# Kernel tuning notes

Measured on AMD Instinct MI355X. Metric: run time of the kernel, lower is better.

## Reference

```python
import jax, jax.numpy as jnp
import numpy as np

D_MODEL = 512
NUM_HEADS = 8
D_K = D_MODEL // NUM_HEADS
SCALE = D_K ** (-0.5)
B, L = 2, 256


def _tropical_linear(x, W, b):
    # max-plus linear: y[..., o] = max_i (x[..., i] + W[o, i]) + b[o]
    # x: (B, L, Din), W: (Dout, Din)
    return jnp.max(x[:, :, None, :] + W[None, None, :, :], axis=-1) + b


def _split_heads(t):
    Bn, Ln, Dn = t.shape
    return t.reshape(Bn, Ln, NUM_HEADS, D_K).transpose(0, 2, 1, 3)  # (B,H,L,dk)


def setup_inputs() -> dict:
    key = jax.random.key(0)
    ks = jax.random.split(key, 8)
    s = 1.0 / np.sqrt(D_MODEL)
    return {
        "x": jax.random.normal(ks[0], (B, L, D_MODEL), jnp.float32),
        "qW": jax.random.normal(ks[1], (D_MODEL, D_MODEL), jnp.float32) * s,
        "qb": jnp.zeros((D_MODEL,), jnp.float32),
        "kW": jax.random.normal(ks[2], (D_MODEL, D_MODEL), jnp.float32) * s,
        "kb": jnp.zeros((D_MODEL,), jnp.float32),
        "vW": jax.random.normal(ks[3], (D_MODEL, D_MODEL), jnp.float32) * s,
        "vb": jnp.zeros((D_MODEL,), jnp.float32),
        "oW": jax.random.normal(ks[4], (D_MODEL, D_MODEL), jnp.float32) * s,
        "ob": jnp.zeros((D_MODEL,), jnp.float32),
        "gW": jnp.zeros((NUM_HEADS, D_MODEL), jnp.float32),  # torch init: zeros
        "gb": jnp.full((NUM_HEADS,), 2.0, jnp.float32),      # torch init: +2.0
        "temp": jnp.ones((NUM_HEADS,), jnp.float32),
    }


def reference(x, qW, qb, kW, kb, vW, vb, oW, ob, gW, gb, temp):
    Bn, Ln, Dn = x.shape
    Q = _split_heads(_tropical_linear(x, qW, qb))  # (B,H,L,dk)
    K = _split_heads(_tropical_linear(x, kW, kb))
    V = _split_heads(x @ vW.T + vb)

    class_scores = jnp.einsum('bhqd,bhkd->bhqk', Q, K) * SCALE
    # tropical max-plus scores: max_d (Q[q,d] + K[k,d])
    trop_scores = jnp.max(Q[:, :, :, None, :] + K[:, :, None, :, :], axis=-1) * SCALE

    g = jax.nn.sigmoid(x @ gW.T + gb)            # (B,L,H)
    g = g.transpose(0, 2, 1)[..., None]          # (B,H,L,1)
    scores = g * trop_scores + (1.0 - g) * class_scores

    # Maslov temperature softmax: per-head learnable temperature
    attn = jax.nn.softmax(scores / temp[None, :, None, None], axis=-1)

    out = jnp.einsum('bhqk,bhkd->bhqd', attn, V)
    out = out.transpose(0, 2, 1, 3).reshape(Bn, Ln, Dn)
    return out @ oW.T + ob, attn
```

## Files before the change

### kernel.cpp

```cpp
#include <hip/hip_runtime.h>
#include <math.h>

#define DM    512
#define LSEQ  256
#define NB    2
#define NH    8
#define DK    64
#define SCALEF 0.125f
#define KC    64

__global__ __launch_bounds__(256) void qkvg_kernel(
    const float* __restrict__ x,
    const float* __restrict__ qW, const float* __restrict__ kW,
    const float* __restrict__ vW,
    const float* __restrict__ gW, const float* __restrict__ gb,
    float* __restrict__ P1, float* __restrict__ go)
{
    const int tid = threadIdx.x;
    const int bx  = blockIdx.x;

    if (bx >= 768) {
        const int gx  = bx - 768;
        const int row = gx * 32 + (tid >> 3);
        const int h   = tid & 7;
        const float4* xr = (const float4*)(x  + row * DM);
        const float4* wr = (const float4*)(gW + h  * DM);
        float acc = 0.f;
        #pragma unroll 8
        for (int i = 0; i < DM / 4; ++i) {
            float4 a = xr[i], w = wr[i];
            acc = fmaf(a.x, w.x, acc);
            acc = fmaf(a.y, w.y, acc);
            acc = fmaf(a.z, w.z, acc);
            acc = fmaf(a.w, w.w, acc);
        }
        acc += gb[h];
        go[row * NH + h] = 1.f / (1.f + __expf(-acc));
        return;
    }

    const int ks = bx & 3;
    const int t  = bx >> 2;
    const int rt = t / 24;
    const int ct = t % 24;
    const int op = ct >> 3;
    const int row0  = rt * 64;
    const int col0m = (ct & 7) * 64;
    const int kbase = ks * 128;

    const float* __restrict__ W = (op == 0) ? qW : (op == 1) ? kW : vW;
    const bool trop = (op < 2);

    __shared__ float Xs[KC][68];
    __shared__ float Ws[KC][68];

    const int ty = tid >> 4, tx = tid & 15;
    const int sr = tid & 63;
    const int sq = tid >> 6;

    const float* xp = x + (row0  + sr) * DM + kbase + sq * 16;
    const float* wp = W + (col0m + sr) * DM + kbase + sq * 16;

    float4 xg[4], wg[4];
    #pragma unroll
    for (int i = 0; i < 4; ++i) {
        xg[i] = *(const float4*)(xp + i * 4);
        wg[i] = *(const float4*)(wp + i * 4);
    }

    const float init = trop ? -INFINITY : 0.f;
    float acc[4][4];
    #pragma unroll
    for (int i = 0; i < 4; ++i)
        #pragma unroll
        for (int j = 0; j < 4; ++j) acc[i][j] = init;

    #pragma unroll
    for (int k0 = 0; k0 < 128; k0 += KC) {
        __syncthreads();
        #pragma unroll
        for (int i = 0; i < 4; ++i) {
            const int kk = sq * 16 + i * 4;
            Xs[kk + 0][sr] = xg[i].x;  Xs[kk + 1][sr] = xg[i].y;
            Xs[kk + 2][sr] = xg[i].z;  Xs[kk + 3][sr] = xg[i].w;
            Ws[kk + 0][sr] = wg[i].x;  Ws[kk + 1][sr] = wg[i].y;
            Ws[kk + 2][sr] = wg[i].z;  Ws[kk + 3][sr] = wg[i].w;
        }
        __syncthreads();
        if (k0 + KC < 128) {
            #pragma unroll
            for (int i = 0; i < 4; ++i) {
                xg[i] = *(const float4*)(xp + KC + i * 4);
                wg[i] = *(const float4*)(wp + KC + i * 4);
            }
        }
        if (trop) {
            #pragma unroll 4
            for (int kp = 0; kp < KC / 2; ++kp) {
                const int kk = kp * 2;
                float4 x0 = *(const float4*)&Xs[kk    ][ty * 4];
                float4 x1 = *(const float4*)&Xs[kk + 1][ty * 4];
                float4 w0 = *(const float4*)&Ws[kk    ][tx * 4];
                float4 w1 = *(const float4*)&Ws[kk + 1][tx * 4];
                const float xa0[4] = {x0.x, x0.y, x0.z, x0.w};
                const float xa1[4] = {x1.x, x1.y, x1.z, x1.w};
                const float wa0[4] = {w0.x, w0.y, w0.z, w0.w};
                const float wa1[4] = {w1.x, w1.y, w1.z, w1.w};
                #pragma unroll
                for (int i = 0; i < 4; ++i)
                    #pragma unroll
                    for (int j = 0; j < 4; ++j)
                        acc[i][j] = fmaxf(fmaxf(acc[i][j], xa0[i] + wa0[j]),
                                          xa1[i] + wa1[j]);
            }
        } else {
            #pragma unroll 4
            for (int kp = 0; kp < KC / 2; ++kp) {
                const int kk = kp * 2;
                float4 x0 = *(const float4*)&Xs[kk    ][ty * 4];
                float4 x1 = *(const float4*)&Xs[kk + 1][ty * 4];
                float4 w0 = *(const float4*)&Ws[kk    ][tx * 4];
                float4 w1 = *(const float4*)&Ws[kk + 1][tx * 4];
                const float xa0[4] = {x0.x, x0.y, x0.z, x0.w};
                const float xa1[4] = {x1.x, x1.y, x1.z, x1.w};
                const float wa0[4] = {w0.x, w0.y, w0.z, w0.w};
                const float wa1[4] = {w1.x, w1.y, w1.z, w1.w};
                #pragma unroll
                for (int i = 0; i < 4; ++i)
                    #pragma unroll
                    for (int j = 0; j < 4; ++j) {
                        acc[i][j] = fmaf(xa0[i], wa0[j], acc[i][j]);
                        acc[i][j] = fmaf(xa1[i], wa1[j], acc[i][j]);
                    }
            }
        }
    }

    const int gcol = op * 512 + col0m + tx * 4;
    #pragma unroll
    for (int i = 0; i < 4; ++i) {
        const int r = row0 + ty * 4 + i;
        *(float4*)&P1[((size_t)ks * 512 + r) * 1536 + gcol] =
            make_float4(acc[i][0], acc[i][1], acc[i][2], acc[i][3]);
    }
}

__global__ __launch_bounds__(256) void qkv_reduce_kernel(
    const float* __restrict__ P1,
    const float* __restrict__ qb, const float* __restrict__ kb,
    const float* __restrict__ vb,
    float* __restrict__ Qo, float* __restrict__ Ko, float* __restrict__ Vo)
{
    const int e   = blockIdx.x * 256 + threadIdx.x;
    const int row = e / 384;
    const int col = (e % 384) * 4;
    const size_t base = (size_t)row * 1536 + col;

    float4 p0 = *(const float4*)&P1[base];
    float4 p1 = *(const float4*)&P1[base +  786432];
    float4 p2 = *(const float4*)&P1[base + 1572864];
    float4 p3 = *(const float4*)&P1[base + 2359296];

    if (col < 1024) {
        float4 r = make_float4(
            fmaxf(fmaxf(p0.x, p1.x), fmaxf(p2.x, p3.x)),
            fmaxf(fmaxf(p0.y, p1.y), fmaxf(p2.y, p3.y)),
            fmaxf(fmaxf(p0.z, p1.z), fmaxf(p2.z, p3.z)),
            fmaxf(fmaxf(p0.w, p1.w), fmaxf(p2.w, p3.w)));
        if (col < 512) {
            float4 b = *(const float4*)&qb[col];
            r.x += b.x; r.y += b.y; r.z += b.z; r.w += b.w;
            *(float4*)&Qo[(size_t)row * DM + col] = r;
        } else {
            float4 b = *(const float4*)&kb[col - 512];
            r.x += b.x; r.y += b.y; r.z += b.z; r.w += b.w;
            *(float4*)&Ko[(size_t)row * DM + col - 512] = r;
        }
    } else {
        float4 b = *(const float4*)&vb[col - 1024];
        float4 r = make_float4(p0.x + p1.x + p2.x + p3.x + b.x,
                               p0.y + p1.y + p2.y + p3.y + b.y,
                               p0.z + p1.z + p2.z + p3.z + b.z,
                               p0.w + p1.w + p2.w + p3.w + b.w);
        *(float4*)&Vo[(size_t)row * DM + col - 1024] = r;
    }
}

__global__ __launch_bounds__(512) void attn_kernel(
    const float* __restrict__ Q, const float* __restrict__ K,
    const float* __restrict__ V, const float* __restrict__ g,
    const float* __restrict__ temp,
    float* __restrict__ attn_out, float* __restrict__ hout)
{
    const int tid = threadIdx.x;
    const int bh  = blockIdx.y;
    const int b   = bh >> 3, h = bh & 7;
    const int q0  = blockIdx.x * 16;
    const int ty  = tid >> 5;
    const int tx  = tid & 31;

    __shared__ float Qs[16][68];
    __shared__ float Kd[64][68];
    __shared__ float Vs[2][64][68];
    __shared__ float Ss[16][260];

    if (tid < 256) {
        const int r = tid >> 4, c = (tid & 15) * 4;
        *(float4*)&Qs[r][c] =
            *(const float4*)&Q[(size_t)(b * LSEQ + q0 + r) * DM + h * DK + c];
    }
    const float gq   = g[(b * LSEQ + q0 + ty) * NH + h];
    const float invt = SCALEF / temp[h];

    const int sr = tid & 63;
    const int sq = tid >> 6;

    for (int kt = 0; kt < 4; ++kt) {
        __syncthreads();
        {
            const float* kp = K + (size_t)(b * LSEQ + kt * 64 + sr) * DM
                              + h * DK + sq * 8;
            #pragma unroll
            for (int i = 0; i < 2; ++i) {
                float4 v = *(const float4*)(kp + i * 4);
                const int d = sq * 8 + i * 4;
                Kd[d + 0][sr] = v.x;  Kd[d + 1][sr] = v.y;
                Kd[d + 2][sr] = v.z;  Kd[d + 3][sr] = v.w;
            }
        }
        __syncthreads();
        float d0 = 0.f, d1 = 0.f;
        float t0 = -INFINITY, t1 = -INFINITY;
        #pragma unroll
        for (int k4 = 0; k4 < 16; ++k4) {
            const float4 q4 = *(const float4*)&Qs[ty][k4 * 4];
            float2 ka = *(const float2*)&Kd[k4 * 4 + 0][tx * 2];
            float2 kb = *(const float2*)&Kd[k4 * 4 + 1][tx * 2];
            float2 kc = *(const float2*)&Kd[k4 * 4 + 2][tx * 2];
            float2 kd = *(const float2*)&Kd[k4 * 4 + 3][tx * 2];
            d0 = fmaf(q4.x, ka.x, d0); d0 = fmaf(q4.y, kb.x, d0);
            d0 = fmaf(q4.z, kc.x, d0); d0 = fmaf(q4.w, kd.x, d0);
            d1 = fmaf(q4.x, ka.y, d1); d1 = fmaf(q4.y, kb.y, d1);
            d1 = fmaf(q4.z, kc.y, d1); d1 = fmaf(q4.w, kd.y, d1);
            t0 = fmaxf(fmaxf(t0, q4.x + ka.x), q4.y + kb.x);
            t0 = fmaxf(fmaxf(t0, q4.z + kc.x), q4.w + kd.x);
            t1 = fmaxf(fmaxf(t1, q4.x + ka.y), q4.y + kb.y);
            t1 = fmaxf(fmaxf(t1, q4.z + kc.y), q4.w + kd.y);
        }
        const float gi = 1.f - gq;
        *(float2*)&Ss[ty][kt * 64 + tx * 2] = make_float2(
            (gq * t0 + gi * d0) * invt, (gq * t1 + gi * d1) * invt);
    }
    __syncthreads();

    {
        float m = -INFINITY;
        #pragma unroll
        for (int j = 0; j < 8; ++j) m = fmaxf(m, Ss[ty][tx + 32 * j]);
        #pragma unroll
        for (int o = 16; o; o >>= 1) m = fmaxf(m, __shfl_xor(m, o));
        float s = 0.f;
        #pragma unroll
        for (int j = 0; j < 8; ++j) {
            const float e = __expf(Ss[ty][tx + 32 * j] - m);
            Ss[ty][tx + 32 * j] = e;
            s += e;
        }
        #pragma unroll
        for (int o = 16; o; o >>= 1) s += __shfl_xor(s, o);
        const float rs = 1.f / s;
        #pragma unroll
        for (int j = 0; j < 8; ++j) Ss[ty][tx + 32 * j] *= rs;
    }
    __syncthreads();

    {
        float* dst = attn_out + (size_t)(bh * LSEQ + q0) * LSEQ;
        #pragma unroll
        for (int i = 0; i < 2; ++i) {
            const int f   = i * 2048 + tid * 4;
            const int row = f >> 8, col = f & 255;
            *(float4*)&dst[f] = *(const float4*)&Ss[row][col];
        }
    }

    const int kh = tid >> 8;
    const int bb = tid & 255;
    const int r  = bb >> 4;
    const int d4 = bb & 15;
    float o0 = 0.f, o1 = 0.f, o2 = 0.f, o3 = 0.f;

    const int vr    = tid & 63;
    const int vslot = tid >> 6;

    for (int p = 0; p < 2; ++p) {
        __syncthreads();
        {
            const int tile = vslot >> 2;
            const int tidx = tile ? (2 + p) : p;
            const float* vp = V + (size_t)(b * LSEQ + tidx * 64 + vr) * DM
                              + h * DK + (vslot & 3) * 16;
            #pragma unroll
            for (int i = 0; i < 4; ++i)
                *(float4*)&Vs[tile][vr][(vslot & 3) * 16 + i * 4] =
                    *(const float4*)(vp + i * 4);
        }
        __syncthreads();
        const int kt = kh * 2 + p;
        #pragma unroll 4
        for (int k4 = 0; k4 < 16; ++k4) {
            float4 a  = *(const float4*)&Ss[r][kt * 64 + k4 * 4];
            float4 v0 = *(const float4*)&Vs[kh][k4 * 4 + 0][d4 * 4];
            float4 v1 = *(const float4*)&Vs[kh][k4 * 4 + 1][d4 * 4];
            float4 v2 = *(const float4*)&Vs[kh][k4 * 4 + 2][d4 * 4];
            float4 v3 = *(const float4*)&Vs[kh][k4 * 4 + 3][d4 * 4];
            o0 = fmaf(a.x, v0.x, o0); o0 = fmaf(a.y, v1.x, o0);
            o0 = fmaf(a.z, v2.x, o0); o0 = fmaf(a.w, v3.x, o0);
            o1 = fmaf(a.x, v0.y, o1); o1 = fmaf(a.y, v1.y, o1);
            o1 = fmaf(a.z, v2.y, o1); o1 = fmaf(a.w, v3.y, o1);
            o2 = fmaf(a.x, v0.z, o2); o2 = fmaf(a.y, v1.z, o2);
            o2 = fmaf(a.z, v2.z, o2); o2 = fmaf(a.w, v3.z, o2);
            o3 = fmaf(a.x, v0.w, o3); o3 = fmaf(a.y, v1.w, o3);
            o3 = fmaf(a.z, v2.w, o3); o3 = fmaf(a.w, v3.w, o3);
        }
    }
    __syncthreads();
    if (kh == 1)
        *(float4*)&Kd[r][d4 * 4] = make_float4(o0, o1, o2, o3);
    __syncthreads();
    if (kh == 0) {
        float4 po = *(const float4*)&Kd[r][d4 * 4];
        *(float4*)&hout[(size_t)(b * LSEQ + q0 + r) * DM + h * DK + d4 * 4] =
            make_float4(o0 + po.x, o1 + po.y, o2 + po.z, o3 + po.w);
    }
}

__global__ __launch_bounds__(256) void oproj_kernel(
    const float* __restrict__ hout,
    const float* __restrict__ oW,
    float* __restrict__ P2)
{
    const int tid = threadIdx.x;
    const int bx  = blockIdx.x;
    const int ks  = bx & 7;
    const int t   = bx >> 3;
    const int row0 = (t >> 3) * 64;
    const int col0 = (t & 7) * 64;
    const int kbase = ks * 64;

    __shared__ float Xs[KC][68];
    __shared__ float Ws[KC][68];

    const int ty = tid >> 4, tx = tid & 15;
    const int sr = tid & 63;
    const int sq = tid >> 6;

    {
        const float* xp = hout + (size_t)(row0 + sr) * DM + kbase + sq * 16;
        const float* wp = oW   + (size_t)(col0 + sr) * DM + kbase + sq * 16;
        #pragma unroll
        for (int i = 0; i < 4; ++i) {
            float4 xv = *(const float4*)(xp + i * 4);
            float4 wv = *(const float4*)(wp + i * 4);
            const int kk = sq * 16 + i * 4;
            Xs[kk + 0][sr] = xv.x;  Xs[kk + 1][sr] = xv.y;
            Xs[kk + 2][sr] = xv.z;  Xs[kk + 3][sr] = xv.w;
            Ws[kk + 0][sr] = wv.x;  Ws[kk + 1][sr] = wv.y;
            Ws[kk + 2][sr] = wv.z;  Ws[kk + 3][sr] = wv.w;
        }
    }
    __syncthreads();

    float acc[4][4] = {};
    #pragma unroll 4
    for (int kp = 0; kp < KC / 2; ++kp) {
        const int kk = kp * 2;
        float4 x0 = *(const float4*)&Xs[kk    ][ty * 4];
        float4 x1 = *(const float4*)&Xs[kk + 1][ty * 4];
        float4 w0 = *(const float4*)&Ws[kk    ][tx * 4];
        float4 w1 = *(const float4*)&Ws[kk + 1][tx * 4];
        const float xa0[4] = {x0.x, x0.y, x0.z, x0.w};
        const float xa1[4] = {x1.x, x1.y, x1.z, x1.w};
        const float wa0[4] = {w0.x, w0.y, w0.z, w0.w};
        const float wa1[4] = {w1.x, w1.y, w1.z, w1.w};
        #pragma unroll
        for (int i = 0; i < 4; ++i)
            #pragma unroll
            for (int j = 0; j < 4; ++j) {
                acc[i][j] = fmaf(xa0[i], wa0[j], acc[i][j]);
                acc[i][j] = fmaf(xa1[i], wa1[j], acc[i][j]);
            }
    }

    #pragma unroll
    for (int i = 0; i < 4; ++i) {
        const int r = row0 + ty * 4 + i;
        *(float4*)&P2[((size_t)ks * 512 + r) * 512 + col0 + tx * 4] =
            make_float4(acc[i][0], acc[i][1], acc[i][2], acc[i][3]);
    }
}

__global__ __launch_bounds__(256) void oproj_reduce_kernel(
    const float* __restrict__ P2, const float* __restrict__ ob,
    float* __restrict__ out)
{
    const int e   = blockIdx.x * 256 + threadIdx.x;
    const int row = e >> 7;
    const int col = (e & 127) * 4;
    const size_t base = (size_t)row * 512 + col;

    float4 b = *(const float4*)&ob[col];
    float4 r = b;
    #pragma unroll
    for (int s = 0; s < 8; ++s) {
        float4 p = *(const float4*)&P2[base + (size_t)s * 262144];
        r.x += p.x; r.y += p.y; r.z += p.z; r.w += p.w;
    }
    *(float4*)&out[base] = r;
}

extern "C" void kernel_launch(void* const* d_in, const int* in_sizes, int n_in,
                              void* d_out, int out_size, void* d_ws, size_t ws_size,
                              hipStream_t stream)
{
    const float* x    = (const float*)d_in[0];
    const float* qW   = (const float*)d_in[1];
    const float* qb   = (const float*)d_in[2];
    const float* kW   = (const float*)d_in[3];
    const float* kb   = (const float*)d_in[4];
    const float* vW   = (const float*)d_in[5];
    const float* vb   = (const float*)d_in[6];
    const float* oW   = (const float*)d_in[7];
    const float* ob   = (const float*)d_in[8];
    const float* gW   = (const float*)d_in[9];
    const float* gb   = (const float*)d_in[10];
    const float* temp = (const float*)d_in[11];

    float* out      = (float*)d_out;
    float* attn_out = out + NB * LSEQ * DM;

    float* ws   = (float*)d_ws;
    float* Qo   = ws;
    float* Ko   = Qo + NB * LSEQ * DM;
    float* Vo   = Ko + NB * LSEQ * DM;
    float* go   = Vo + NB * LSEQ * DM;
    float* hout = go + NB * LSEQ * NH;
    float* P1   = hout + NB * LSEQ * DM;
    float* P2   = P1;

    qkvg_kernel<<<dim3(784), 256, 0, stream>>>(
        x, qW, kW, vW, gW, gb, P1, go);
    qkv_reduce_kernel<<<dim3(768), 256, 0, stream>>>(
        P1, qb, kb, vb, Qo, Ko, Vo);
    attn_kernel<<<dim3(16, 16), 512, 0, stream>>>(
        Qo, Ko, Vo, go, temp, attn_out, hout);
    oproj_kernel<<<dim3(512), 256, 0, stream>>>(
        hout, oW, P2);
    oproj_reduce_kernel<<<dim3(256), 256, 0, stream>>>(
        P2, ob, out);
}
```

Measured before the change: 141.6 us.

## Enlarge projection tiles to 128x128 with 8x8 register blocking and deeper split-K

The QKV and output projection GEMMs move from 64x64 tiles with 4x4 per-thread outputs to 128x128 tiles with 8x8 per-thread outputs. Weights are stored pair-interleaved in shared memory so each lane fetches them with wide loads. Split-K doubles (8 and 16 partials), so the reduce kernels read more partial buffers. The attention kernel keeps Q rows in registers, reuses the shared buffers, and splits the PV product four ways with a shared-memory combine. The aim is less shared-memory traffic per FLOP, at the cost of more register pressure, fewer blocks, and larger partial-sum reductions.

```diff
diff --git a/kernel.cpp b/kernel.cpp
--- a/kernel.cpp
+++ b/kernel.cpp
@@ -7,7 +7,6 @@
 #define NH    8
 #define DK    64
 #define SCALEF 0.125f
-#define KC    64
 
 __global__ __launch_bounds__(256) void qkvg_kernel(
     const float* __restrict__ x,
@@ -19,8 +18,8 @@
     const int tid = threadIdx.x;
     const int bx  = blockIdx.x;
 
-    if (bx >= 768) {
-        const int gx  = bx - 768;
+    if (bx >= 384) {
+        const int gx  = bx - 384;
         const int row = gx * 32 + (tid >> 3);
         const int h   = tid & 7;
         const float4* xr = (const float4*)(x  + row * DM);
@@ -39,109 +38,93 @@
         return;
     }
 
-    const int ks = bx & 3;
-    const int t  = bx >> 2;
-    const int rt = t / 24;
-    const int ct = t % 24;
-    const int op = ct >> 3;
-    const int row0  = rt * 64;
-    const int col0m = (ct & 7) * 64;
-    const int kbase = ks * 128;
+    const int ks = bx & 7;
+    const int t  = bx >> 3;
+    const int rt = t / 12;
+    const int ct = t % 12;
+    const int op = ct >> 2;
+    const int row0  = rt * 128;
+    const int col0m = (ct & 3) * 128;
+    const int kbase = ks * 64;
 
     const float* __restrict__ W = (op == 0) ? qW : (op == 1) ? kW : vW;
     const bool trop = (op < 2);
 
-    __shared__ float Xs[KC][68];
-    __shared__ float Ws[KC][68];
+    __shared__ float Xs[64][128];
+    __shared__ float Wp[32][256];
+
+    const int sr = tid & 127;
+    const int sq = tid >> 7;
+
+    {
+        const float* xp = x + (size_t)(row0  + sr) * DM + kbase + sq * 32;
+        const float* wp = W + (size_t)(col0m + sr) * DM + kbase + sq * 32;
+        #pragma unroll
+        for (int i = 0; i < 8; ++i) {
+            float4 xv = *(const float4*)(xp + i * 4);
+            float4 wv = *(const float4*)(wp + i * 4);
+            const int kk = sq * 32 + i * 4;
+            Xs[kk + 0][sr] = xv.x;  Xs[kk + 1][sr] = xv.y;
+            Xs[kk + 2][sr] = xv.z;  Xs[kk + 3][sr] = xv.w;
+            const int kp = (kk >> 1);
+            *(float2*)&Wp[kp    ][2 * sr] = make_float2(wv.x, wv.y);
+            *(float2*)&Wp[kp + 1][2 * sr] = make_float2(wv.z, wv.w);
+        }
+    }
+    __syncthreads();
 
     const int ty = tid >> 4, tx = tid & 15;
-    const int sr = tid & 63;
-    const int sq = tid >> 6;
-
-    const float* xp = x + (row0  + sr) * DM + kbase + sq * 16;
-    const float* wp = W + (col0m + sr) * DM + kbase + sq * 16;
-
-    float4 xg[4], wg[4];
-    #pragma unroll
-    for (int i = 0; i < 4; ++i) {
-        xg[i] = *(const float4*)(xp + i * 4);
-        wg[i] = *(const float4*)(wp + i * 4);
-    }
-
     const float init = trop ? -INFINITY : 0.f;
-    float acc[4][4];
-    #pragma unroll
-    for (int i = 0; i < 4; ++i)
-        #pragma unroll
-        for (int j = 0; j < 4; ++j) acc[i][j] = init;
-
-    #pragma unroll
-    for (int k0 = 0; k0 < 128; k0 += KC) {
-        __syncthreads();
-        #pragma unroll
-        for (int i = 0; i < 4; ++i) {
-            const int kk = sq * 16 + i * 4;
-            Xs[kk + 0][sr] = xg[i].x;  Xs[kk + 1][sr] = xg[i].y;
-            Xs[kk + 2][sr] = xg[i].z;  Xs[kk + 3][sr] = xg[i].w;
-            Ws[kk + 0][sr] = wg[i].x;  Ws[kk + 1][sr] = wg[i].y;
-            Ws[kk + 2][sr] = wg[i].z;  Ws[kk + 3][sr] = wg[i].w;
-        }
-        __syncthreads();
-        if (k0 + KC < 128) {
+    float acc[8][8];
+    #pragma unroll
+    for (int i = 0; i < 8; ++i)
+        #pragma unroll
+        for (int j = 0; j < 8; ++j) acc[i][j] = init;
+
+    #pragma unroll 2
+    for (int kp = 0; kp < 32; ++kp) {
+        const int kk = kp * 2;
+        const float4 xa0 = *(const float4*)&Xs[kk    ][ty * 8];
+        const float4 xa1 = *(const float4*)&Xs[kk    ][ty * 8 + 4];
+        const float4 xb0 = *(const float4*)&Xs[kk + 1][ty * 8];
+        const float4 xb1 = *(const float4*)&Xs[kk + 1][ty * 8 + 4];
+        const float4 wq[4] = {
+            *(const float4*)&Wp[kp][tx * 16     ],
+            *(const float4*)&Wp[kp][tx * 16 +  4],
+            *(const float4*)&Wp[kp][tx * 16 +  8],
+            *(const float4*)&Wp[kp][tx * 16 + 12] };
+        const float x0[8] = {xa0.x,xa0.y,xa0.z,xa0.w,xa1.x,xa1.y,xa1.z,xa1.w};
+        const float x1[8] = {xb0.x,xb0.y,xb0.z,xb0.w,xb1.x,xb1.y,xb1.z,xb1.w};
+        if (trop) {
             #pragma unroll
-            for (int i = 0; i < 4; ++i) {
-                xg[i] = *(const float4*)(xp + KC + i * 4);
-                wg[i] = *(const float4*)(wp + KC + i * 4);
-            }
-        }
-        if (trop) {
-            #pragma unroll 4
-            for (int kp = 0; kp < KC / 2; ++kp) {
-                const int kk = kp * 2;
-                float4 x0 = *(const float4*)&Xs[kk    ][ty * 4];
-                float4 x1 = *(const float4*)&Xs[kk + 1][ty * 4];
-                float4 w0 = *(const float4*)&Ws[kk    ][tx * 4];
-                float4 w1 = *(const float4*)&Ws[kk + 1][tx * 4];
-                const float xa0[4] = {x0.x, x0.y, x0.z, x0.w};
-                const float xa1[4] = {x1.x, x1.y, x1.z, x1.w};
-                const float wa0[4] = {w0.x, w0.y, w0.z, w0.w};
-                const float wa1[4] = {w1.x, w1.y, w1.z, w1.w};
+            for (int i = 0; i < 4; ++i)
                 #pragma unroll
-                for (int i = 0; i < 4; ++i)
-                    #pragma unroll
-                    for (int j = 0; j < 4; ++j)
-                        acc[i][j] = fmaxf(fmaxf(acc[i][j], xa0[i] + wa0[j]),
-                                          xa1[i] + wa1[j]);
-            }
+                for (int r = 0; r < 8; ++r) {
+                    acc[r][2*i  ] = fmaxf(fmaxf(acc[r][2*i  ], x0[r]+wq[i].x),
+                                          x1[r]+wq[i].y);
+                    acc[r][2*i+1] = fmaxf(fmaxf(acc[r][2*i+1], x0[r]+wq[i].z),
+                                          x1[r]+wq[i].w);
+                }
         } else {
-            #pragma unroll 4
-            for (int kp = 0; kp < KC / 2; ++kp) {
-                const int kk = kp * 2;
-                float4 x0 = *(const float4*)&Xs[kk    ][ty * 4];
-                float4 x1 = *(const float4*)&Xs[kk + 1][ty * 4];
-                float4 w0 = *(const float4*)&Ws[kk    ][tx * 4];
-                float4 w1 = *(const float4*)&Ws[kk + 1][tx * 4];
-                const float xa0[4] = {x0.x, x0.y, x0.z, x0.w};
-                const float xa1[4] = {x1.x, x1.y, x1.z, x1.w};
-                const float wa0[4] = {w0.x, w0.y, w0.z, w0.w};
-                const float wa1[4] = {w1.x, w1.y, w1.z, w1.w};
+            #pragma unroll
+            for (int i = 0; i < 4; ++i)
                 #pragma unroll
-                for (int i = 0; i < 4; ++i)
-                    #pragma unroll
-                    for (int j = 0; j < 4; ++j) {
-                        acc[i][j] = fmaf(xa0[i], wa0[j], acc[i][j]);
-                        acc[i][j] = fmaf(xa1[i], wa1[j], acc[i][j]);
-                    }
-            }
-        }
-    }
-
-    const int gcol = op * 512 + col0m + tx * 4;
-    #pragma unroll
-    for (int i = 0; i < 4; ++i) {
-        const int r = row0 + ty * 4 + i;
-        *(float4*)&P1[((size_t)ks * 512 + r) * 1536 + gcol] =
-            make_float4(acc[i][0], acc[i][1], acc[i][2], acc[i][3]);
+                for (int r = 0; r < 8; ++r) {
+                    acc[r][2*i  ] = fmaf(x0[r], wq[i].x, acc[r][2*i  ]);
+                    acc[r][2*i  ] = fmaf(x1[r], wq[i].y, acc[r][2*i  ]);
+                    acc[r][2*i+1] = fmaf(x0[r], wq[i].z, acc[r][2*i+1]);
+                    acc[r][2*i+1] = fmaf(x1[r], wq[i].w, acc[r][2*i+1]);
+                }
+        }
+    }
+
+    const int gcol = op * 512 + col0m + tx * 8;
+    #pragma unroll
+    for (int r = 0; r < 8; ++r) {
+        const int grow = row0 + ty * 8 + r;
+        float* dst = &P1[((size_t)ks * 512 + grow) * 1536 + gcol];
+        *(float4*)dst       = make_float4(acc[r][0], acc[r][1], acc[r][2], acc[r][3]);
+        *(float4*)(dst + 4) = make_float4(acc[r][4], acc[r][5], acc[r][6], acc[r][7]);
     }
 }
 
@@ -156,17 +139,18 @@
     const int col = (e % 384) * 4;
     const size_t base = (size_t)row * 1536 + col;
 
-    float4 p0 = *(const float4*)&P1[base];
-    float4 p1 = *(const float4*)&P1[base +  786432];
-    float4 p2 = *(const float4*)&P1[base + 1572864];
-    float4 p3 = *(const float4*)&P1[base + 2359296];
+    float4 p[8];
+    #pragma unroll
+    for (int s = 0; s < 8; ++s)
+        p[s] = *(const float4*)&P1[base + (size_t)s * 786432];
 
     if (col < 1024) {
-        float4 r = make_float4(
-            fmaxf(fmaxf(p0.x, p1.x), fmaxf(p2.x, p3.x)),
-            fmaxf(fmaxf(p0.y, p1.y), fmaxf(p2.y, p3.y)),
-            fmaxf(fmaxf(p0.z, p1.z), fmaxf(p2.z, p3.z)),
-            fmaxf(fmaxf(p0.w, p1.w), fmaxf(p2.w, p3.w)));
+        float4 r = p[0];
+        #pragma unroll
+        for (int s = 1; s < 8; ++s) {
+            r.x = fmaxf(r.x, p[s].x); r.y = fmaxf(r.y, p[s].y);
+            r.z = fmaxf(r.z, p[s].z); r.w = fmaxf(r.w, p[s].w);
+        }
         if (col < 512) {
             float4 b = *(const float4*)&qb[col];
             r.x += b.x; r.y += b.y; r.z += b.z; r.w += b.w;
@@ -178,10 +162,11 @@
         }
     } else {
         float4 b = *(const float4*)&vb[col - 1024];
-        float4 r = make_float4(p0.x + p1.x + p2.x + p3.x + b.x,
-                               p0.y + p1.y + p2.y + p3.y + b.y,
-                               p0.z + p1.z + p2.z + p3.z + b.z,
-                               p0.w + p1.w + p2.w + p3.w + b.w);
+        float4 r = b;
+        #pragma unroll
+        for (int s = 0; s < 8; ++s) {
+            r.x += p[s].x; r.y += p[s].y; r.z += p[s].z; r.w += p[s].w;
+        }
         *(float4*)&Vo[(size_t)row * DM + col - 1024] = r;
     }
 }
@@ -199,33 +184,32 @@
     const int ty  = tid >> 5;
     const int tx  = tid & 31;
 
-    __shared__ float Qs[16][68];
-    __shared__ float Kd[64][68];
-    __shared__ float Vs[2][64][68];
+    __shared__ float As[64][68];
+    __shared__ float Bs[64][68];
     __shared__ float Ss[16][260];
 
-    if (tid < 256) {
-        const int r = tid >> 4, c = (tid & 15) * 4;
-        *(float4*)&Qs[r][c] =
-            *(const float4*)&Q[(size_t)(b * LSEQ + q0 + r) * DM + h * DK + c];
-    }
+    const float* qrow = Q + (size_t)(b * LSEQ + q0 + ty) * DM + h * DK;
+    float4 qreg[16];
+    #pragma unroll
+    for (int i = 0; i < 16; ++i) qreg[i] = *(const float4*)(qrow + i * 4);
+
     const float gq   = g[(b * LSEQ + q0 + ty) * NH + h];
     const float invt = SCALEF / temp[h];
 
-    const int sr = tid & 63;
-    const int sq = tid >> 6;
+    const int ksr = tid & 63;
+    const int ksq = tid >> 6;
 
     for (int kt = 0; kt < 4; ++kt) {
         __syncthreads();
         {
-            const float* kp = K + (size_t)(b * LSEQ + kt * 64 + sr) * DM
-                              + h * DK + sq * 8;
+            const float* kp = K + (size_t)(b * LSEQ + kt * 64 + ksr) * DM
+                              + h * DK + ksq * 8;
             #pragma unroll
             for (int i = 0; i < 2; ++i) {
                 float4 v = *(const float4*)(kp + i * 4);
-                const int d = sq * 8 + i * 4;
-                Kd[d + 0][sr] = v.x;  Kd[d + 1][sr] = v.y;
-                Kd[d + 2][sr] = v.z;  Kd[d + 3][sr] = v.w;
+                const int d = ksq * 8 + i * 4;
+                As[d + 0][ksr] = v.x;  As[d + 1][ksr] = v.y;
+                As[d + 2][ksr] = v.z;  As[d + 3][ksr] = v.w;
             }
         }
         __syncthreads();
@@ -233,11 +217,11 @@
         float t0 = -INFINITY, t1 = -INFINITY;
         #pragma unroll
         for (int k4 = 0; k4 < 16; ++k4) {
-            const float4 q4 = *(const float4*)&Qs[ty][k4 * 4];
-            float2 ka = *(const float2*)&Kd[k4 * 4 + 0][tx * 2];
-            float2 kb = *(const float2*)&Kd[k4 * 4 + 1][tx * 2];
-            float2 kc = *(const float2*)&Kd[k4 * 4 + 2][tx * 2];
-            float2 kd = *(const float2*)&Kd[k4 * 4 + 3][tx * 2];
+            const float4 q4 = qreg[k4];
+            float2 ka = *(const float2*)&As[k4 * 4 + 0][tx * 2];
+            float2 kb = *(const float2*)&As[k4 * 4 + 1][tx * 2];
+            float2 kc = *(const float2*)&As[k4 * 4 + 2][tx * 2];
+            float2 kd = *(const float2*)&As[k4 * 4 + 3][tx * 2];
             d0 = fmaf(q4.x, ka.x, d0); d0 = fmaf(q4.y, kb.x, d0);
             d0 = fmaf(q4.z, kc.x, d0); d0 = fmaf(q4.w, kd.x, d0);
             d1 = fmaf(q4.x, ka.y, d1); d1 = fmaf(q4.y, kb.y, d1);
@@ -284,54 +268,77 @@
         }
     }
 
-    const int kh = tid >> 8;
-    const int bb = tid & 255;
-    const int r  = bb >> 4;
-    const int d4 = bb & 15;
-    float o0 = 0.f, o1 = 0.f, o2 = 0.f, o3 = 0.f;
-
+    const int g4 = tid >> 7;
+    const int kh = g4 >> 1, kq = g4 & 1;
+    const int rp = (tid >> 4) & 7;
+    const int d4 = tid & 15;
+    float o00=0.f,o01=0.f,o02=0.f,o03=0.f;
+    float o10=0.f,o11=0.f,o12=0.f,o13=0.f;
+
+    const int vtile = tid >> 8;
     const int vr    = tid & 63;
-    const int vslot = tid >> 6;
+    const int vw    = (tid >> 6) & 3;
 
     for (int p = 0; p < 2; ++p) {
         __syncthreads();
         {
-            const int tile = vslot >> 2;
-            const int tidx = tile ? (2 + p) : p;
-            const float* vp = V + (size_t)(b * LSEQ + tidx * 64 + vr) * DM
-                              + h * DK + (vslot & 3) * 16;
+            const int tsrc = vtile ? (2 + p) : p;
+            const float* vp = V + (size_t)(b * LSEQ + tsrc * 64 + vr) * DM
+                              + h * DK + vw * 16;
+            float* vdst = vtile ? &Bs[vr][vw * 16] : &As[vr][vw * 16];
             #pragma unroll
             for (int i = 0; i < 4; ++i)
-                *(float4*)&Vs[tile][vr][(vslot & 3) * 16 + i * 4] =
-                    *(const float4*)(vp + i * 4);
+                *(float4*)(vdst + i * 4) = *(const float4*)(vp + i * 4);
         }
         __syncthreads();
         const int kt = kh * 2 + p;
+        const float* vb = kh ? &Bs[0][0] : &As[0][0];
+        const int koff = kt * 64 + kq * 32;
         #pragma unroll 4
-        for (int k4 = 0; k4 < 16; ++k4) {
-            float4 a  = *(const float4*)&Ss[r][kt * 64 + k4 * 4];
-            float4 v0 = *(const float4*)&Vs[kh][k4 * 4 + 0][d4 * 4];
-            float4 v1 = *(const float4*)&Vs[kh][k4 * 4 + 1][d4 * 4];
-            float4 v2 = *(const float4*)&Vs[kh][k4 * 4 + 2][d4 * 4];
-            float4 v3 = *(const float4*)&Vs[kh][k4 * 4 + 3][d4 * 4];
-            o0 = fmaf(a.x, v0.x, o0); o0 = fmaf(a.y, v1.x, o0);
-            o0 = fmaf(a.z, v2.x, o0); o0 = fmaf(a.w, v3.x, o0);
-            o1 = fmaf(a.x, v0.y, o1); o1 = fmaf(a.y, v1.y, o1);
-            o1 = fmaf(a.z, v2.y, o1); o1 = fmaf(a.w, v3.y, o1);
-            o2 = fmaf(a.x, v0.z, o2); o2 = fmaf(a.y, v1.z, o2);
-            o2 = fmaf(a.z, v2.z, o2); o2 = fmaf(a.w, v3.z, o2);
-            o3 = fmaf(a.x, v0.w, o3); o3 = fmaf(a.y, v1.w, o3);
-            o3 = fmaf(a.z, v2.w, o3); o3 = fmaf(a.w, v3.w, o3);
-        }
-    }
-    __syncthreads();
-    if (kh == 1)
-        *(float4*)&Kd[r][d4 * 4] = make_float4(o0, o1, o2, o3);
-    __syncthreads();
-    if (kh == 0) {
-        float4 po = *(const float4*)&Kd[r][d4 * 4];
-        *(float4*)&hout[(size_t)(b * LSEQ + q0 + r) * DM + h * DK + d4 * 4] =
-            make_float4(o0 + po.x, o1 + po.y, o2 + po.z, o3 + po.w);
+        for (int k4 = 0; k4 < 8; ++k4) {
+            const int kl = kq * 32 + k4 * 4;
+            float4 a0 = *(const float4*)&Ss[rp * 2    ][koff + k4 * 4];
+            float4 a1 = *(const float4*)&Ss[rp * 2 + 1][koff + k4 * 4];
+            float4 v0 = *(const float4*)&vb[(kl    ) * 68 + d4 * 4];
+            float4 v1 = *(const float4*)&vb[(kl + 1) * 68 + d4 * 4];
+            float4 v2 = *(const float4*)&vb[(kl + 2) * 68 + d4 * 4];
+            float4 v3 = *(const float4*)&vb[(kl + 3) * 68 + d4 * 4];
+            o00 = fmaf(a0.x, v0.x, o00); o00 = fmaf(a0.y, v1.x, o00);
+            o00 = fmaf(a0.z, v2.x, o00); o00 = fmaf(a0.w, v3.x, o00);
+            o01 = fmaf(a0.x, v0.y, o01); o01 = fmaf(a0.y, v1.y, o01);
+            o01 = fmaf(a0.z, v2.y, o01); o01 = fmaf(a0.w, v3.y, o01);
+            o02 = fmaf(a0.x, v0.z, o02); o02 = fmaf(a0.y, v1.z, o02);
+            o02 = fmaf(a0.z, v2.z, o02); o02 = fmaf(a0.w, v3.z, o02);
+            o03 = fmaf(a0.x, v0.w, o03); o03 = fmaf(a0.y, v1.w, o03);
+            o03 = fmaf(a0.z, v2.w, o03); o03 = fmaf(a0.w, v3.w, o03);
+            o10 = fmaf(a1.x, v0.x, o10); o10 = fmaf(a1.y, v1.x, o10);
+            o10 = fmaf(a1.z, v2.x, o10); o10 = fmaf(a1.w, v3.x, o10);
+            o11 = fmaf(a1.x, v0.y, o11); o11 = fmaf(a1.y, v1.y, o11);
+            o11 = fmaf(a1.z, v2.y, o11); o11 = fmaf(a1.w, v3.y, o11);
+            o12 = fmaf(a1.x, v0.z, o12); o12 = fmaf(a1.y, v1.z, o12);
+            o12 = fmaf(a1.z, v2.z, o12); o12 = fmaf(a1.w, v3.z, o12);
+            o13 = fmaf(a1.x, v0.w, o13); o13 = fmaf(a1.y, v1.w, o13);
+            o13 = fmaf(a1.z, v2.w, o13); o13 = fmaf(a1.w, v3.w, o13);
+        }
+    }
+    __syncthreads();
+    if (g4 > 0) {
+        const int cr = (g4 - 1) * 16 + rp * 2;
+        *(float4*)&As[cr    ][d4 * 4] = make_float4(o00, o01, o02, o03);
+        *(float4*)&As[cr + 1][d4 * 4] = make_float4(o10, o11, o12, o13);
+    }
+    __syncthreads();
+    if (g4 == 0) {
+        #pragma unroll
+        for (int s = 0; s < 3; ++s) {
+            float4 p0 = *(const float4*)&As[s * 16 + rp * 2    ][d4 * 4];
+            float4 p1 = *(const float4*)&As[s * 16 + rp * 2 + 1][d4 * 4];
+            o00 += p0.x; o01 += p0.y; o02 += p0.z; o03 += p0.w;
+            o10 += p1.x; o11 += p1.y; o12 += p1.z; o13 += p1.w;
+        }
+        const size_t r0 = (size_t)(b * LSEQ + q0 + rp * 2) * DM + h * DK + d4 * 4;
+        *(float4*)&hout[r0]      = make_float4(o00, o01, o02, o03);
+        *(float4*)&hout[r0 + DM] = make_float4(o10, o11, o12, o13);
     }
 }
 
@@ -342,18 +349,17 @@
 {
     const int tid = threadIdx.x;
     const int bx  = blockIdx.x;
-    const int ks  = bx & 7;
-    const int t   = bx >> 3;
-    const int row0 = (t >> 3) * 64;
-    const int col0 = (t & 7) * 64;
-    const int kbase = ks * 64;
-
-    __shared__ float Xs[KC][68];
-    __shared__ float Ws[KC][68];
-
-    const int ty = tid >> 4, tx = tid & 15;
-    const int sr = tid & 63;
-    const int sq = tid >> 6;
+    const int ks  = bx & 15;
+    const int t   = bx >> 4;
+    const int row0 = (t >> 2) * 128;
+    const int col0 = (t & 3) * 128;
+    const int kbase = ks * 32;
+
+    __shared__ float Xs[32][128];
+    __shared__ float Wp[16][256];
+
+    const int sr = tid & 127;
+    const int sq = tid >> 7;
 
     {
         const float* xp = hout + (size_t)(row0 + sr) * DM + kbase + sq * 16;
@@ -365,38 +371,47 @@
             const int kk = sq * 16 + i * 4;
             Xs[kk + 0][sr] = xv.x;  Xs[kk + 1][sr] = xv.y;
             Xs[kk + 2][sr] = xv.z;  Xs[kk + 3][sr] = xv.w;
-            Ws[kk + 0][sr] = wv.x;  Ws[kk + 1][sr] = wv.y;
-            Ws[kk + 2][sr] = wv.z;  Ws[kk + 3][sr] = wv.w;
-        }
-    }
-    __syncthreads();
-
-    float acc[4][4] = {};
-    #pragma unroll 4
-    for (int kp = 0; kp < KC / 2; ++kp) {
+            const int kp = (kk >> 1);
+            *(float2*)&Wp[kp    ][2 * sr] = make_float2(wv.x, wv.y);
+            *(float2*)&Wp[kp + 1][2 * sr] = make_float2(wv.z, wv.w);
+        }
+    }
+    __syncthreads();
+
+    const int ty = tid >> 4, tx = tid & 15;
+    float acc[8][8] = {};
+
+    #pragma unroll 2
+    for (int kp = 0; kp < 16; ++kp) {
         const int kk = kp * 2;
-        float4 x0 = *(const float4*)&Xs[kk    ][ty * 4];
-        float4 x1 = *(const float4*)&Xs[kk + 1][ty * 4];
-        float4 w0 = *(const float4*)&Ws[kk    ][tx * 4];
-        float4 w1 = *(const float4*)&Ws[kk + 1][tx * 4];
-        const float xa0[4] = {x0.x, x0.y, x0.z, x0.w};
-        const float xa1[4] = {x1.x, x1.y, x1.z, x1.w};
-        const float wa0[4] = {w0.x, w0.y, w0.z, w0.w};
-        const float wa1[4] = {w1.x, w1.y, w1.z, w1.w};
+        const float4 xa0 = *(const float4*)&Xs[kk    ][ty * 8];
+        const float4 xa1 = *(const float4*)&Xs[kk    ][ty * 8 + 4];
+        const float4 xb0 = *(const float4*)&Xs[kk + 1][ty * 8];
+        const float4 xb1 = *(const float4*)&Xs[kk + 1][ty * 8 + 4];
+        const float4 wq[4] = {
+            *(const float4*)&Wp[kp][tx * 16     ],
+            *(const float4*)&Wp[kp][tx * 16 +  4],
+            *(const float4*)&Wp[kp][tx * 16 +  8],
+            *(const float4*)&Wp[kp][tx * 16 + 12] };
+        const float x0[8] = {xa0.x,xa0.y,xa0.z,xa0.w,xa1.x,xa1.y,xa1.z,xa1.w};
+        const float x1[8] = {xb0.x,xb0.y,xb0.z,xb0.w,xb1.x,xb1.y,xb1.z,xb1.w};
         #pragma unroll
         for (int i = 0; i < 4; ++i)
             #pragma unroll
-            for (int j = 0; j < 4; ++j) {
-                acc[i][j] = fmaf(xa0[i], wa0[j], acc[i][j]);
-                acc[i][j] = fmaf(xa1[i], wa1[j], acc[i][j]);
+            for (int r = 0; r < 8; ++r) {
+                acc[r][2*i  ] = fmaf(x0[r], wq[i].x, acc[r][2*i  ]);
+                acc[r][2*i  ] = fmaf(x1[r], wq[i].y, acc[r][2*i  ]);
+                acc[r][2*i+1] = fmaf(x0[r], wq[i].z, acc[r][2*i+1]);
+                acc[r][2*i+1] = fmaf(x1[r], wq[i].w, acc[r][2*i+1]);
             }
     }
 
     #pragma unroll
-    for (int i = 0; i < 4; ++i) {
-        const int r = row0 + ty * 4 + i;
-        *(float4*)&P2[((size_t)ks * 512 + r) * 512 + col0 + tx * 4] =
-            make_float4(acc[i][0], acc[i][1], acc[i][2], acc[i][3]);
+    for (int r = 0; r < 8; ++r) {
+        const int grow = row0 + ty * 8 + r;
+        float* dst = &P2[((size_t)ks * 512 + grow) * 512 + col0 + tx * 8];
+        *(float4*)dst       = make_float4(acc[r][0], acc[r][1], acc[r][2], acc[r][3]);
+        *(float4*)(dst + 4) = make_float4(acc[r][4], acc[r][5], acc[r][6], acc[r][7]);
     }
 }
 
@@ -412,7 +427,7 @@
     float4 b = *(const float4*)&ob[col];
     float4 r = b;
     #pragma unroll
-    for (int s = 0; s < 8; ++s) {
+    for (int s = 0; s < 16; ++s) {
         float4 p = *(const float4*)&P2[base + (size_t)s * 262144];
         r.x += p.x; r.y += p.y; r.z += p.z; r.w += p.w;
     }
@@ -448,13 +463,13 @@
     float* P1   = hout + NB * LSEQ * DM;
     float* P2   = P1;
 
-    qkvg_kernel<<<dim3(784), 256, 0, stream>>>(
+    qkvg_kernel<<<dim3(400), 256, 0, stream>>>(
         x, qW, kW, vW, gW, gb, P1, go);
     qkv_reduce_kernel<<<dim3(768), 256, 0, stream>>>(
         P1, qb, kb, vb, Qo, Ko, Vo);
     attn_kernel<<<dim3(16, 16), 512, 0, stream>>>(
         Qo, Ko, Vo, go, temp, attn_out, hout);
-    oproj_kernel<<<dim3(512), 256, 0, stream>>>(
+    oproj_kernel<<<dim3(256), 256, 0, stream>>>(
         hout, oW, P2);
     oproj_reduce_kernel<<<dim3(256), 256, 0, stream>>>(
         P2, ob, out);
```

After: 145.6 us. 1.03x slower.
